# Kernel optimization log

Measured on AMD Instinct MI355X. Metric: run time of the kernel, lower is better.

The kernel has to match this reference:

```python
import jax, jax.numpy as jnp
import numpy as np

D_MODEL = 128
N_HEADS = 8
D_K = D_MODEL // N_HEADS
N_TGT = 40000
N_SRC = 40000
N_EDGES = 640000


def setup_inputs() -> dict:
    key = jax.random.key(0)
    ks = jax.random.split(key, 12)
    s = 1.0 / np.sqrt(D_MODEL)
    return {
        "X_tgt": jax.random.normal(ks[0], (N_TGT, D_MODEL), jnp.float32),
        "X_src": jax.random.normal(ks[1], (N_SRC, D_MODEL), jnp.float32),
        "inc_tgt": jax.random.randint(ks[2], (N_EDGES,), 0, N_TGT),
        "inc_src": jax.random.randint(ks[3], (N_EDGES,), 0, N_SRC),
        "num_tgt": N_TGT,
        # weights stored (in, out): y = x @ W
        "Wq": jax.random.normal(ks[4], (D_MODEL, D_MODEL), jnp.float32) * s,
        "Wkv": jax.random.normal(ks[5], (D_MODEL, 2 * D_MODEL), jnp.float32) * s,
        "Wbt": jax.random.normal(ks[6], (D_MODEL, N_HEADS), jnp.float32) * s,
        "Wbs": jax.random.normal(ks[7], (D_MODEL, N_HEADS), jnp.float32) * s,
        "Wgt_w": jax.random.normal(ks[8], (D_MODEL, D_MODEL), jnp.float32) * s,
        "Wgt_b": jnp.zeros((D_MODEL,), jnp.float32),
        "Wgs_w": jax.random.normal(ks[9], (D_MODEL, D_MODEL), jnp.float32) * s,
        "Wgs_b": jnp.zeros((D_MODEL,), jnp.float32),
        "Wo": jax.random.normal(ks[10], (D_MODEL, D_MODEL), jnp.float32) * s,
    }


def reference(X_tgt, X_src, inc_tgt, inc_src, num_tgt, Wq, Wkv, Wbt, Wbs,
              Wgt_w, Wgt_b, Wgs_w, Wgs_b, Wo):
    H, dk = N_HEADS, D_K
    scale = 1.0 / np.sqrt(dk)
    n_src = X_src.shape[0]

    Q = (X_tgt @ Wq).reshape(-1, H, dk)                 # [Nt,H,dk]
    kv = (X_src @ Wkv).reshape(n_src, 2, H, dk)
    K, V = kv[:, 0], kv[:, 1]                           # [Ns,H,dk]

    # per-edge attention scores [E,H]
    scores = (jnp.sum(Q[inc_tgt] * K[inc_src], axis=-1) * scale
              + (X_tgt @ Wbt)[inc_tgt]
              + (X_src @ Wbs)[inc_src])

    # segment softmax over edges grouped by target node
    mx = jax.ops.segment_max(scores, inc_tgt, num_segments=num_tgt)  # [Nt,H]
    exp_s = jnp.exp(scores - mx[inc_tgt])
    sm = jax.ops.segment_sum(exp_s, inc_tgt, num_segments=num_tgt)
    attn = exp_s / (sm[inc_tgt] + 1e-12)                # [E,H]

    g_src = jax.nn.sigmoid(X_src @ Wgs_w + Wgs_b).reshape(n_src, H, dk)
    msg = attn[..., None] * (g_src[inc_src] * V[inc_src])          # [E,H,dk]
    out = jax.ops.segment_sum(msg, inc_tgt, num_segments=num_tgt)  # [Nt,H,dk]

    g_tgt = jax.nn.sigmoid(X_tgt @ Wgt_w + Wgt_b).reshape(-1, H, dk)
    return (g_tgt * out).reshape(-1, H * dk) @ Wo
```

## Files before the change

kernel.cpp:

```cpp
#include <hip/hip_runtime.h>
#include <math.h>

#define NTGT 40000
#define NSRC 40000
#define NEDGE 640000
#define LOG2E 1.44269504088896f
#define KGROW 256
#define CAP 64

typedef __attribute__((ext_vector_type(8))) short bfrag;
typedef __attribute__((ext_vector_type(4))) short bhalf4;
typedef __attribute__((ext_vector_type(8))) short bhalf8;
typedef __attribute__((ext_vector_type(4))) float f4acc;

__device__ __forceinline__ ushort f2bf(float f) {
  uint u = __float_as_uint(f);
  u += 0x7fffu + ((u >> 16) & 1u);
  return (ushort)(u >> 16);
}
__device__ __forceinline__ float bflo(uint u) { return __uint_as_float(u << 16); }
__device__ __forceinline__ float bfhi(uint u) { return __uint_as_float(u & 0xffff0000u); }
__device__ __forceinline__ float bf2f(short s) { return __uint_as_float(((uint)(ushort)s) << 16); }
__device__ __forceinline__ float sigmoidf_fast(float x) { return 1.0f / (1.0f + __expf(-x)); }

__global__ __launch_bounds__(256) void k_prep(const float* __restrict__ Wq,
                                              const float* __restrict__ Wkv,
                                              const float* __restrict__ Wgt_w,
                                              const float* __restrict__ Wgs_w,
                                              const float* __restrict__ Wo,
                                              const float* __restrict__ Wbs,
                                              int* __restrict__ cntp,
                                              short* __restrict__ WqT, short* __restrict__ WkT,
                                              short* __restrict__ WvT, short* __restrict__ WgtT,
                                              short* __restrict__ WgsT, short* __restrict__ WoT,
                                              short* __restrict__ WbsT) {
  const int b = blockIdx.x;
  const int tid = threadIdx.x;
  if (b >= 7) {
    int i = (b - 7) * 1024 + tid * 4;
    int4 z = {0, 0, 0, 0};
    *reinterpret_cast<int4*>(cntp + i) = z;
    return;
  }
  if (b == 6) {
    for (int idx = tid; idx < 16 * 128; idx += 256) {
      int n = idx >> 7, k = idx & 127;
      WbsT[idx] = (n < 8) ? (short)f2bf(Wbs[k * 8 + n]) : (short)0;
    }
    return;
  }
  __shared__ short T[128][136];
  const float* src;
  int ld, off;
  short* dst;
  switch (b) {
    case 0: src = Wq;    ld = 128; off = 0;   dst = WqT;  break;
    case 1: src = Wkv;   ld = 256; off = 0;   dst = WkT;  break;
    case 2: src = Wkv;   ld = 256; off = 128; dst = WvT;  break;
    case 3: src = Wgt_w; ld = 128; off = 0;   dst = WgtT; break;
    case 4: src = Wgs_w; ld = 128; off = 0;   dst = WgsT; break;
    default:src = Wo;    ld = 128; off = 0;   dst = WoT;  break;
  }
  for (int i = tid; i < 128 * 32; i += 256) {
    int k = i >> 5, c4 = (i & 31) * 4;
    float4 v = *reinterpret_cast<const float4*>(src + (size_t)k * ld + off + c4);
    T[c4 + 0][k] = (short)f2bf(v.x);
    T[c4 + 1][k] = (short)f2bf(v.y);
    T[c4 + 2][k] = (short)f2bf(v.z);
    T[c4 + 3][k] = (short)f2bf(v.w);
  }
  __syncthreads();
  for (int u = tid; u < 128 * 16; u += 256) {
    int n = u >> 4, o = (u & 15) * 8;
    *reinterpret_cast<bhalf8*>(dst + (size_t)n * 128 + o) =
        *reinterpret_cast<const bhalf8*>(&T[n][o]);
  }
}

__global__ __launch_bounds__(512) void k_fill(const int* __restrict__ inc_tgt,
                                              const int* __restrict__ inc_src,
                                              int* __restrict__ cntp,
                                              ushort* __restrict__ elist) {
  const int tid = threadIdx.x;
  const int part = blockIdx.x & 7;
  const int ebase = (blockIdx.x >> 3) * 2000;
#pragma unroll
  for (int k = 0; k < 4; ++k) {
    int off = k * 512 + tid;
    if (off < 2000) {
      int e = ebase + off;
      int t = inc_tgt[e];
      if ((t & 7) == part) {
        int pos = atomicAdd(&cntp[t << 4], 1);
        pos = min(pos, CAP - 1);
        elist[t * CAP + pos] = (ushort)inc_src[e];
      }
    }
  }
}

#define MFMA16(a, b, c) __builtin_amdgcn_mfma_f32_16x16x32_bf16(a, b, c, 0, 0, 0)

__device__ __forceinline__ void stage_issue(const float* __restrict__ X, size_t row0,
                                            float4 ld[4], int tid) {
#pragma unroll
  for (int it = 0; it < 4; ++it) {
    int i = it * 512 + tid;
    int r = i >> 5, c4 = (i & 31) * 4;
    ld[it] = *reinterpret_cast<const float4*>(X + (row0 + r) * 128 + c4);
  }
}
__device__ __forceinline__ void stage_write(short (*Xs)[136], const float4 ld[4], int tid) {
#pragma unroll
  for (int it = 0; it < 4; ++it) {
    int i = it * 512 + tid;
    int r = i >> 5, c4 = (i & 31) * 4;
    bhalf4 o;
    o[0] = (short)f2bf(ld[it].x); o[1] = (short)f2bf(ld[it].y);
    o[2] = (short)f2bf(ld[it].z); o[3] = (short)f2bf(ld[it].w);
    *reinterpret_cast<bhalf4*>(&Xs[r][c4]) = o;
  }
}

__global__ __launch_bounds__(512) void k_proj(const float* __restrict__ Xt,
                                              const float* __restrict__ Xsrc,
                                              const short* __restrict__ WqT,
                                              const short* __restrict__ WgtT,
                                              const short* __restrict__ WkT,
                                              const short* __restrict__ WvT,
                                              const short* __restrict__ WgsT,
                                              const short* __restrict__ WbsT,
                                              const float* __restrict__ Wgt_b,
                                              const float* __restrict__ Wgs_b,
                                              short* __restrict__ Qb, short* __restrict__ gtb,
                                              short* __restrict__ KG,
                                              short* __restrict__ bsb) {
  const int tid = threadIdx.x;
  __shared__ short Xs[64][136];
  __shared__ short Stg[64][256];
  const int w = tid >> 6, lane = tid & 63;
  const int nl = lane & 15;
  const int kg = (lane >> 4) * 8;
  const int r4 = (lane >> 4) * 4;
  const int c0 = w * 16;
  const bool is_src = blockIdx.x >= 125;
  const int t0 = (is_src ? blockIdx.x - 125 : blockIdx.x) * 5;
  const float* X = is_src ? Xsrc : Xt;

  if (!is_src) {
    bfrag Bq[4], Bg[4];
#pragma unroll
    for (int ks = 0; ks < 4; ++ks) {
      const size_t wo = (size_t)(c0 + nl) * 128 + ks * 32 + kg;
      Bq[ks] = *reinterpret_cast<const bfrag*>(WqT + wo);
      Bg[ks] = *reinterpret_cast<const bfrag*>(WgtT + wo);
    }
    const int c = c0 + nl;
    const float gb = Wgt_b[c];
    {
      float4 ld[4];
      stage_issue(X, (size_t)t0 * 64, ld, tid);
      stage_write(Xs, ld, tid);
    }
    __syncthreads();
    for (int ti = 0; ti < 5; ++ti) {
      const size_t row0 = (size_t)(t0 + ti) * 64;
      float4 ld[4];
      if (ti < 4) stage_issue(X, row0 + 64, ld, tid);
      f4acc aQ[4] = {}, aG[4] = {};
#pragma unroll
      for (int ks = 0; ks < 4; ++ks) {
        const int ko = ks * 32 + kg;
        bfrag a0 = *reinterpret_cast<const bfrag*>(&Xs[nl][ko]);
        bfrag a1 = *reinterpret_cast<const bfrag*>(&Xs[16 + nl][ko]);
        bfrag a2 = *reinterpret_cast<const bfrag*>(&Xs[32 + nl][ko]);
        bfrag a3 = *reinterpret_cast<const bfrag*>(&Xs[48 + nl][ko]);
        aQ[0] = MFMA16(a0, Bq[ks], aQ[0]);
        aQ[1] = MFMA16(a1, Bq[ks], aQ[1]);
        aQ[2] = MFMA16(a2, Bq[ks], aQ[2]);
        aQ[3] = MFMA16(a3, Bq[ks], aQ[3]);
        aG[0] = MFMA16(a0, Bg[ks], aG[0]);
        aG[1] = MFMA16(a1, Bg[ks], aG[1]);
        aG[2] = MFMA16(a2, Bg[ks], aG[2]);
        aG[3] = MFMA16(a3, Bg[ks], aG[3]);
      }
#pragma unroll
      for (int rf = 0; rf < 4; ++rf)
#pragma unroll
        for (int j = 0; j < 4; ++j) {
          int r = rf * 16 + r4 + j;
          Stg[r][c] = (short)f2bf(aQ[rf][j] * (0.25f * LOG2E));
          Stg[r][128 + c] = (short)f2bf(sigmoidf_fast(aG[rf][j] + gb));
        }
      __syncthreads();
      if (ti < 4) stage_write(Xs, ld, tid);
      for (int u = tid; u < 1024; u += 512) {
        int r = u >> 4, o = (u & 15) * 8;
        *reinterpret_cast<bhalf8*>(Qb + (row0 + r) * 128 + o) =
            *reinterpret_cast<const bhalf8*>(&Stg[r][o]);
        *reinterpret_cast<bhalf8*>(gtb + (row0 + r) * 128 + o) =
            *reinterpret_cast<const bhalf8*>(&Stg[r][128 + o]);
      }
      __syncthreads();
    }
  } else {
    bfrag Bk[4], Bv[4], Bg[4], Bb[4];
#pragma unroll
    for (int ks = 0; ks < 4; ++ks) {
      const size_t wo = (size_t)(c0 + nl) * 128 + ks * 32 + kg;
      Bk[ks] = *reinterpret_cast<const bfrag*>(WkT + wo);
      Bv[ks] = *reinterpret_cast<const bfrag*>(WvT + wo);
      Bg[ks] = *reinterpret_cast<const bfrag*>(WgsT + wo);
      Bb[ks] = *reinterpret_cast<const bfrag*>(WbsT + (size_t)nl * 128 + ks * 32 + kg);
    }
    const int c = c0 + nl;
    const int slot = (c >> 1) * 4 + (c & 1);
    const float gb = Wgs_b[c];
    {
      float4 ld[4];
      stage_issue(X, (size_t)t0 * 64, ld, tid);
      stage_write(Xs, ld, tid);
    }
    __syncthreads();
    for (int ti = 0; ti < 5; ++ti) {
      const size_t row0 = (size_t)(t0 + ti) * 64;
      float4 ld[4];
      if (ti < 4) stage_issue(X, row0 + 64, ld, tid);
      f4acc aK[4] = {}, aV[4] = {}, aG[4] = {}, aB[4] = {};
#pragma unroll
      for (int ks = 0; ks < 4; ++ks) {
        const int ko = ks * 32 + kg;
        bfrag a0 = *reinterpret_cast<const bfrag*>(&Xs[nl][ko]);
        bfrag a1 = *reinterpret_cast<const bfrag*>(&Xs[16 + nl][ko]);
        bfrag a2 = *reinterpret_cast<const bfrag*>(&Xs[32 + nl][ko]);
        bfrag a3 = *reinterpret_cast<const bfrag*>(&Xs[48 + nl][ko]);
        aK[0] = MFMA16(a0, Bk[ks], aK[0]);
        aK[1] = MFMA16(a1, Bk[ks], aK[1]);
        aK[2] = MFMA16(a2, Bk[ks], aK[2]);
        aK[3] = MFMA16(a3, Bk[ks], aK[3]);
        aV[0] = MFMA16(a0, Bv[ks], aV[0]);
        aV[1] = MFMA16(a1, Bv[ks], aV[1]);
        aV[2] = MFMA16(a2, Bv[ks], aV[2]);
        aV[3] = MFMA16(a3, Bv[ks], aV[3]);
        aG[0] = MFMA16(a0, Bg[ks], aG[0]);
        aG[1] = MFMA16(a1, Bg[ks], aG[1]);
        aG[2] = MFMA16(a2, Bg[ks], aG[2]);
        aG[3] = MFMA16(a3, Bg[ks], aG[3]);
        if (w == 0) {
          aB[0] = MFMA16(a0, Bb[ks], aB[0]);
          aB[1] = MFMA16(a1, Bb[ks], aB[1]);
          aB[2] = MFMA16(a2, Bb[ks], aB[2]);
          aB[3] = MFMA16(a3, Bb[ks], aB[3]);
        }
      }
#pragma unroll
      for (int rf = 0; rf < 4; ++rf)
#pragma unroll
        for (int j = 0; j < 4; ++j) {
          int r = rf * 16 + r4 + j;
          float g = sigmoidf_fast(aG[rf][j] + gb);
          Stg[r][slot] = (short)f2bf(aK[rf][j]);
          Stg[r][slot + 2] = (short)f2bf(g * aV[rf][j]);
        }
      if (w == 0 && nl < 8) {
#pragma unroll
        for (int rf = 0; rf < 4; ++rf)
#pragma unroll
          for (int j = 0; j < 4; ++j)
            bsb[(row0 + rf * 16 + r4 + j) * 8 + nl] = (short)f2bf(aB[rf][j] * LOG2E);
      }
      __syncthreads();
      if (ti < 4) stage_write(Xs, ld, tid);
      for (int u = tid; u < 2048; u += 512) {
        int r = u >> 5, o = (u & 31) * 8;
        *reinterpret_cast<bhalf8*>(KG + (row0 + r) * KGROW + o) =
            *reinterpret_cast<const bhalf8*>(&Stg[r][o]);
      }
      __syncthreads();
    }
  }
}

__global__ __launch_bounds__(256) void k_attn(const uint2* __restrict__ Qp2,
                                              const uint4* __restrict__ KGp4,
                                              const short* __restrict__ bsb,
                                              const uint2* __restrict__ gtp2,
                                              const int* __restrict__ cntp,
                                              const ushort* __restrict__ elist,
                                              uint2* __restrict__ tmpp2) {
  const int wave = threadIdx.x >> 6;
  const int lane = threadIdx.x & 63;
  const int t = blockIdx.x * 4 + wave;
  const int p = lane & 31;
  const int h = p >> 2;
  const int hi = lane >> 5;

  uint2 qv = Qp2[(size_t)t * 32 + p];
  float q0 = bflo(qv.x), q1 = bfhi(qv.x), q2 = bflo(qv.y), q3 = bfhi(qv.y);
  const int deg = min(cntp[t << 4], CAP);
  const int ebase = t * CAP;

  float ssum = 0.f, a0 = 0.f, a1 = 0.f, a2 = 0.f, a3 = 0.f;
  int i = 0;
  for (; i + 8 <= deg; i += 8) {
    int sv[4];
    uint4 kv[4];
    float bv[4], dd[4];
#pragma unroll
    for (int u = 0; u < 4; ++u) sv[u] = (int)elist[ebase + i + 2 * u + hi];
#pragma unroll
    for (int u = 0; u < 4; ++u) {
      kv[u] = KGp4[(size_t)sv[u] * 32 + p];
      bv[u] = bf2f(bsb[(size_t)sv[u] * 8 + h]);
    }
#pragma unroll
    for (int u = 0; u < 4; ++u)
      dd[u] = q0 * bflo(kv[u].x) + q1 * bfhi(kv[u].x) + q2 * bflo(kv[u].z) + q3 * bfhi(kv[u].z);
#pragma unroll
    for (int u = 0; u < 4; ++u) dd[u] += __shfl_xor(dd[u], 1);
#pragma unroll
    for (int u = 0; u < 4; ++u) dd[u] += __shfl_xor(dd[u], 2);
#pragma unroll
    for (int u = 0; u < 4; ++u) {
      float e = __builtin_amdgcn_exp2f(dd[u] + bv[u]);
      ssum += e;
      a0 = fmaf(e, bflo(kv[u].y), a0);
      a1 = fmaf(e, bfhi(kv[u].y), a1);
      a2 = fmaf(e, bflo(kv[u].w), a2);
      a3 = fmaf(e, bfhi(kv[u].w), a3);
    }
  }
  for (; i < deg; i += 2) {
    int idx = i + hi;
    float pen = 0.f;
    if (idx >= deg) { idx = deg - 1; pen = -1e30f; }
    int s = (int)elist[ebase + idx];
    uint4 kv = KGp4[(size_t)s * 32 + p];
    float bsv = bf2f(bsb[(size_t)s * 8 + h]);
    float d = q0 * bflo(kv.x) + q1 * bfhi(kv.x) + q2 * bflo(kv.z) + q3 * bfhi(kv.z);
    d += __shfl_xor(d, 1);
    d += __shfl_xor(d, 2);
    float e = __builtin_amdgcn_exp2f(d + bsv + pen);
    ssum += e;
    a0 = fmaf(e, bflo(kv.y), a0);
    a1 = fmaf(e, bfhi(kv.y), a1);
    a2 = fmaf(e, bflo(kv.w), a2);
    a3 = fmaf(e, bfhi(kv.w), a3);
  }
  ssum += __shfl_xor(ssum, 32);
  a0 += __shfl_xor(a0, 32);
  a1 += __shfl_xor(a1, 32);
  a2 += __shfl_xor(a2, 32);
  a3 += __shfl_xor(a3, 32);
  if (lane < 32) {
    float inv = 1.f / (ssum + 1e-12f);
    uint2 g2 = gtp2[(size_t)t * 32 + p];
    float o0 = bflo(g2.x) * a0 * inv;
    float o1 = bfhi(g2.x) * a1 * inv;
    float o2 = bflo(g2.y) * a2 * inv;
    float o3 = bfhi(g2.y) * a3 * inv;
    uint2 pk;
    pk.x = ((uint)f2bf(o0)) | (((uint)f2bf(o1)) << 16);
    pk.y = ((uint)f2bf(o2)) | (((uint)f2bf(o3)) << 16);
    tmpp2[(size_t)t * 32 + p] = pk;
  }
}

__device__ __forceinline__ void stage_rows_bf16(const short* __restrict__ X, size_t row0,
                                                short (*Xs)[136], int tid) {
  for (int i = tid; i < 64 * 32; i += 256) {
    int r = i >> 5, c4 = (i & 31) * 4;
    *reinterpret_cast<bhalf4*>(&Xs[r][c4]) =
        *reinterpret_cast<const bhalf4*>(X + (row0 + r) * 128 + c4);
  }
}

__device__ __forceinline__ void mfma_pass(const short (*Xs)[136], int wave, int lane,
                                          const short* __restrict__ WT, f4acc acc[8]) {
  const int rl = wave * 16 + (lane & 15);
  const int kg = (lane >> 4) * 8;
  const int nl = lane & 15;
#pragma unroll
  for (int ks = 0; ks < 4; ++ks) {
    bfrag a = *reinterpret_cast<const bfrag*>(&Xs[rl][ks * 32 + kg]);
#pragma unroll
    for (int nf = 0; nf < 8; ++nf) {
      bfrag b = *reinterpret_cast<const bfrag*>(WT + (size_t)(nf * 16 + nl) * 128 + ks * 32 + kg);
      acc[nf] = MFMA16(a, b, acc[nf]);
    }
  }
}

__global__ __launch_bounds__(256) void k_out(const short* __restrict__ tmpb,
                                             const short* __restrict__ WoT,
                                             float* __restrict__ out) {
  __shared__ short Xs[64][136];
  const int tid = threadIdx.x;
  const size_t row0 = (size_t)blockIdx.x * 64;
  stage_rows_bf16(tmpb, row0, Xs, tid);
  __syncthreads();
  const int wave = tid >> 6, lane = tid & 63;
  const int rbase = (int)row0 + wave * 16 + ((lane >> 4) << 2);
  const int cl = lane & 15;
  f4acc acc[8] = {};
  mfma_pass(Xs, wave, lane, WoT, acc);
#pragma unroll
  for (int nf = 0; nf < 8; ++nf)
#pragma unroll
    for (int j = 0; j < 4; ++j)
      out[(size_t)(rbase + j) * 128 + nf * 16 + cl] = acc[nf][j];
}

extern "C" void kernel_launch(void* const* d_in, const int* in_sizes, int n_in,
                              void* d_out, int out_size, void* d_ws, size_t ws_size,
                              hipStream_t stream) {
  const float* X_tgt = (const float*)d_in[0];
  const float* X_src = (const float*)d_in[1];
  const int* inc_tgt = (const int*)d_in[2];
  const int* inc_src = (const int*)d_in[3];
  const float* Wq    = (const float*)d_in[5];
  const float* Wkv   = (const float*)d_in[6];
  const float* Wbs   = (const float*)d_in[8];
  const float* Wgt_w = (const float*)d_in[9];
  const float* Wgt_b = (const float*)d_in[10];
  const float* Wgs_w = (const float*)d_in[11];
  const float* Wgs_b = (const float*)d_in[12];
  const float* Wo    = (const float*)d_in[13];
  float* out = (float*)d_out;

  char* ws = (char*)d_ws;
  short* Qb   = (short*)ws; ws += (size_t)NTGT * 128 * 2;
  short* KG   = (short*)ws; ws += (size_t)NSRC * KGROW * 2;
  short* gtb  = (short*)ws; ws += (size_t)NTGT * 128 * 2;
  short* tmpb = (short*)ws; ws += (size_t)NTGT * 128 * 2;
  short* bsb  = (short*)ws; ws += (size_t)NSRC * 8 * 2;
  int* cntp  = (int*)ws; ws += (size_t)NTGT * 16 * 4;
  ushort* elist = (ushort*)ws; ws += (size_t)NTGT * CAP * 2;
  short* WqT  = (short*)ws; ws += 128 * 128 * 2;
  short* WkT  = (short*)ws; ws += 128 * 128 * 2;
  short* WvT  = (short*)ws; ws += 128 * 128 * 2;
  short* WgtT = (short*)ws; ws += 128 * 128 * 2;
  short* WgsT = (short*)ws; ws += 128 * 128 * 2;
  short* WoT  = (short*)ws; ws += 128 * 128 * 2;
  short* WbsT = (short*)ws; ws += 16 * 128 * 2;

  k_prep<<<632, 256, 0, stream>>>(Wq, Wkv, Wgt_w, Wgs_w, Wo, Wbs, cntp,
                                  WqT, WkT, WvT, WgtT, WgsT, WoT, WbsT);
  k_fill<<<2560, 512, 0, stream>>>(inc_tgt, inc_src, cntp, elist);
  k_proj<<<250, 512, 0, stream>>>(X_tgt, X_src, WqT, WgtT, WkT, WvT, WgsT,
                                  WbsT, Wgt_b, Wgs_b, Qb, gtb, KG, bsb);
  k_attn<<<NTGT / 4, 256, 0, stream>>>((const uint2*)Qb, (const uint4*)KG, bsb,
                                       (const uint2*)gtb, cntp, elist, (uint2*)tmpb);
  k_out<<<NTGT / 64, 256, 0, stream>>>(tmpb, WoT, out);
}
```

Baseline: 128.0 us.

## Double-buffer X and staging tiles in projection kernel to drop a barrier

Adds a second shared-memory buffer for the input tile and the output staging tile in k_proj. The copy-out of the previous tile now runs after the current tile's MFMA and epilogue, and the next tile is written to the alternate buffer, so each loop iteration needs one __syncthreads instead of two. Shared memory per block doubles to roughly 100KB, which may lower occupancy on the 512-thread blocks.

After: 128.4 us. Within noise of the previous version (+0.3%).

```diff
diff --git a/kernel.cpp b/kernel.cpp
--- a/kernel.cpp
+++ b/kernel.cpp
@@ -136,8 +136,8 @@
                                               short* __restrict__ KG,
                                               short* __restrict__ bsb) {
   const int tid = threadIdx.x;
-  __shared__ short Xs[64][136];
-  __shared__ short Stg[64][256];
+  __shared__ short Xs[2][64][136];
+  __shared__ short Stg[2][64][256];
   const int w = tid >> 6, lane = tid & 63;
   const int nl = lane & 15;
   const int kg = (lane >> 4) * 8;
@@ -160,9 +160,10 @@
     {
       float4 ld[4];
       stage_issue(X, (size_t)t0 * 64, ld, tid);
-      stage_write(Xs, ld, tid);
+      stage_write(Xs[0], ld, tid);
     }
     __syncthreads();
+    int cur = 0;
     for (int ti = 0; ti < 5; ++ti) {
       const size_t row0 = (size_t)(t0 + ti) * 64;
       float4 ld[4];
@@ -171,10 +172,10 @@
 #pragma unroll
       for (int ks = 0; ks < 4; ++ks) {
         const int ko = ks * 32 + kg;
-        bfrag a0 = *reinterpret_cast<const bfrag*>(&Xs[nl][ko]);
-        bfrag a1 = *reinterpret_cast<const bfrag*>(&Xs[16 + nl][ko]);
-        bfrag a2 = *reinterpret_cast<const bfrag*>(&Xs[32 + nl][ko]);
-        bfrag a3 = *reinterpret_cast<const bfrag*>(&Xs[48 + nl][ko]);
+        bfrag a0 = *reinterpret_cast<const bfrag*>(&Xs[cur][nl][ko]);
+        bfrag a1 = *reinterpret_cast<const bfrag*>(&Xs[cur][16 + nl][ko]);
+        bfrag a2 = *reinterpret_cast<const bfrag*>(&Xs[cur][32 + nl][ko]);
+        bfrag a3 = *reinterpret_cast<const bfrag*>(&Xs[cur][48 + nl][ko]);
         aQ[0] = MFMA16(a0, Bq[ks], aQ[0]);
         aQ[1] = MFMA16(a1, Bq[ks], aQ[1]);
         aQ[2] = MFMA16(a2, Bq[ks], aQ[2]);
@@ -189,19 +190,32 @@
 #pragma unroll
         for (int j = 0; j < 4; ++j) {
           int r = rf * 16 + r4 + j;
-          Stg[r][c] = (short)f2bf(aQ[rf][j] * (0.25f * LOG2E));
-          Stg[r][128 + c] = (short)f2bf(sigmoidf_fast(aG[rf][j] + gb));
+          Stg[cur][r][c] = (short)f2bf(aQ[rf][j] * (0.25f * LOG2E));
+          Stg[cur][r][128 + c] = (short)f2bf(sigmoidf_fast(aG[rf][j] + gb));
         }
+      if (ti > 0) {
+        const size_t rp = (size_t)(t0 + ti - 1) * 64;
+        for (int u = tid; u < 1024; u += 512) {
+          int r = u >> 4, o = (u & 15) * 8;
+          *reinterpret_cast<bhalf8*>(Qb + (rp + r) * 128 + o) =
+              *reinterpret_cast<const bhalf8*>(&Stg[cur ^ 1][r][o]);
+          *reinterpret_cast<bhalf8*>(gtb + (rp + r) * 128 + o) =
+              *reinterpret_cast<const bhalf8*>(&Stg[cur ^ 1][r][128 + o]);
+        }
+      }
+      if (ti < 4) stage_write(Xs[cur ^ 1], ld, tid);
       __syncthreads();
-      if (ti < 4) stage_write(Xs, ld, tid);
+      cur ^= 1;
+    }
+    {
+      const size_t rp = (size_t)(t0 + 4) * 64;
       for (int u = tid; u < 1024; u += 512) {
         int r = u >> 4, o = (u & 15) * 8;
-        *reinterpret_cast<bhalf8*>(Qb + (row0 + r) * 128 + o) =
-            *reinterpret_cast<const bhalf8*>(&Stg[r][o]);
-        *reinterpret_cast<bhalf8*>(gtb + (row0 + r) * 128 + o) =
-            *reinterpret_cast<const bhalf8*>(&Stg[r][128 + o]);
-      }
-      __syncthreads();
+        *reinterpret_cast<bhalf8*>(Qb + (rp + r) * 128 + o) =
+            *reinterpret_cast<const bhalf8*>(&Stg[cur ^ 1][r][o]);
+        *reinterpret_cast<bhalf8*>(gtb + (rp + r) * 128 + o) =
+            *reinterpret_cast<const bhalf8*>(&Stg[cur ^ 1][r][128 + o]);
+      }
     }
   } else {
     bfrag Bk[4], Bv[4], Bg[4], Bb[4];
@@ -219,9 +233,10 @@
     {
       float4 ld[4];
       stage_issue(X, (size_t)t0 * 64, ld, tid);
-      stage_write(Xs, ld, tid);
+      stage_write(Xs[0], ld, tid);
     }
     __syncthreads();
+    int cur = 0;
     for (int ti = 0; ti < 5; ++ti) {
       const size_t row0 = (size_t)(t0 + ti) * 64;
       float4 ld[4];
@@ -230,10 +245,10 @@
 #pragma unroll
       for (int ks = 0; ks < 4; ++ks) {
         const int ko = ks * 32 + kg;
-        bfrag a0 = *reinterpret_cast<const bfrag*>(&Xs[nl][ko]);
-        bfrag a1 = *reinterpret_cast<const bfrag*>(&Xs[16 + nl][ko]);
-        bfrag a2 = *reinterpret_cast<const bfrag*>(&Xs[32 + nl][ko]);
-        bfrag a3 = *reinterpret_cast<const bfrag*>(&Xs[48 + nl][ko]);
+        bfrag a0 = *reinterpret_cast<const bfrag*>(&Xs[cur][nl][ko]);
+        bfrag a1 = *reinterpret_cast<const bfrag*>(&Xs[cur][16 + nl][ko]);
+        bfrag a2 = *reinterpret_cast<const bfrag*>(&Xs[cur][32 + nl][ko]);
+        bfrag a3 = *reinterpret_cast<const bfrag*>(&Xs[cur][48 + nl][ko]);
         aK[0] = MFMA16(a0, Bk[ks], aK[0]);
         aK[1] = MFMA16(a1, Bk[ks], aK[1]);
         aK[2] = MFMA16(a2, Bk[ks], aK[2]);
@@ -259,8 +274,8 @@
         for (int j = 0; j < 4; ++j) {
           int r = rf * 16 + r4 + j;
           float g = sigmoidf_fast(aG[rf][j] + gb);
-          Stg[r][slot] = (short)f2bf(aK[rf][j]);
-          Stg[r][slot + 2] = (short)f2bf(g * aV[rf][j]);
+          Stg[cur][r][slot] = (short)f2bf(aK[rf][j]);
+          Stg[cur][r][slot + 2] = (short)f2bf(g * aV[rf][j]);
         }
       if (w == 0 && nl < 8) {
 #pragma unroll
@@ -269,14 +284,25 @@
           for (int j = 0; j < 4; ++j)
             bsb[(row0 + rf * 16 + r4 + j) * 8 + nl] = (short)f2bf(aB[rf][j] * LOG2E);
       }
+      if (ti > 0) {
+        const size_t rp = (size_t)(t0 + ti - 1) * 64;
+        for (int u = tid; u < 2048; u += 512) {
+          int r = u >> 5, o = (u & 31) * 8;
+          *reinterpret_cast<bhalf8*>(KG + (rp + r) * KGROW + o) =
+              *reinterpret_cast<const bhalf8*>(&Stg[cur ^ 1][r][o]);
+        }
+      }
+      if (ti < 4) stage_write(Xs[cur ^ 1], ld, tid);
       __syncthreads();
-      if (ti < 4) stage_write(Xs, ld, tid);
+      cur ^= 1;
+    }
+    {
+      const size_t rp = (size_t)(t0 + 4) * 64;
       for (int u = tid; u < 2048; u += 512) {
         int r = u >> 5, o = (u & 31) * 8;
-        *reinterpret_cast<bhalf8*>(KG + (row0 + r) * KGROW + o) =
-            *reinterpret_cast<const bhalf8*>(&Stg[r][o]);
-      }
-      __syncthreads();
+        *reinterpret_cast<bhalf8*>(KG + (rp + r) * KGROW + o) =
+            *reinterpret_cast<const bhalf8*>(&Stg[cur ^ 1][r][o]);
+      }
     }
   }
 }
```
